# Kernel tuning notes

Measured on AMD Instinct MI355X. Metric: run time of the kernel, lower is better.

The kernel has to match this reference:

```python
import jax, jax.numpy as jnp
import numpy as np

N_NODES = 50000
N_EDGES = 1_600_000
F = 64      # num_edge_features
NH = 3      # n_h hidden blocks
BN_EPS = 1e-5


def setup_inputs() -> dict:
    key = jax.random.key(0)
    ks = jax.random.split(key, 8)
    edge_attr = jax.random.normal(ks[0], (N_EDGES, F), jnp.float32)
    nbr_shift = 0.1 * jax.random.normal(ks[1], (N_EDGES, 3), jnp.float32)
    pos = 10.0 * jax.random.normal(ks[2], (N_NODES, 3), jnp.float32)
    edge_index = jax.random.randint(ks[3], (2, N_EDGES), 0, N_NODES, dtype=jnp.int64)
    Ws = jax.random.normal(ks[4], (NH, F, F), jnp.float32) / np.sqrt(F).astype(np.float32)
    bs = jnp.zeros((NH, F), jnp.float32)
    gammas = jnp.ones((NH, F), jnp.float32)
    betas = jnp.zeros((NH, F), jnp.float32)
    w_out = jax.random.normal(ks[5], (F,), jnp.float32) / np.sqrt(F).astype(np.float32)
    b_out = jnp.zeros((1,), jnp.float32)
    return {"edge_attr": edge_attr, "nbr_shift": nbr_shift, "pos": pos,
            "Ws": Ws, "bs": bs, "gammas": gammas, "betas": betas,
            "w_out": w_out, "b_out": b_out, "edge_index": edge_index}


def _batchnorm(x, gamma, beta):
    # training-mode BatchNorm1d: batch mean / biased variance over edges
    mu = jnp.mean(x, axis=0)
    var = jnp.mean(jnp.square(x - mu), axis=0)
    return gamma * (x - mu) * jax.lax.rsqrt(var + BN_EPS) + beta


def reference(edge_attr, nbr_shift, pos, Ws, bs, gammas, betas, w_out, b_out, edge_index):
    j = edge_index[0]  # source atoms
    i = edge_index[1]  # target atoms
    # gather positions by edge, normalized edge direction  [E,3]
    edge_dir = pos[i] + nbr_shift - pos[j]
    edge_len = jnp.sqrt(jnp.sum(jnp.square(edge_dir), axis=-1, keepdims=True))
    edge_dir = edge_dir / edge_len
    h = edge_attr
    for l in range(NH):
        h = _batchnorm(h @ Ws[l] + bs[l], gammas[l], betas[l])
        h = jax.nn.softplus(h)
    s = (h @ w_out)[:, None] + b_out  # [E,1] scalar per edge
    force_e = s * edge_dir            # [E,3]
    # scatter-add edge forces onto target atoms
    force = jax.ops.segment_sum(force_e, i, num_segments=N_NODES)  # [N,3]
    return force
```

## Files before the change

### kernel.cpp

```cpp
#include <hip/hip_runtime.h>
#include <hip/hip_bf16.h>
#include <math.h>

#define F 64
#define TPB 256
#define MTILE 256
#define BN_EPS 1e-5f
#define LGRID 512

typedef __attribute__((ext_vector_type(8))) short short8;
typedef __attribute__((ext_vector_type(4))) float f32x4;

__device__ __forceinline__ float sp(float x) {
    return fmaxf(x, 0.f) + __logf(1.f + __expf(-fabsf(x)));
}
__device__ __forceinline__ ushort f2bf(float f) {
    __hip_bfloat16 h = __float2bfloat16(f);
    return *reinterpret_cast<ushort*>(&h);
}
__device__ __forceinline__ float bf2f(ushort u) {
    unsigned v = ((unsigned)u) << 16;
    return __builtin_bit_cast(float, v);
}

template <int HAS_ACT>
__global__ __launch_bounds__(TPB, 2)
void layer_mfma(const void* __restrict__ Xv, uint2* __restrict__ Yg,
                const float* __restrict__ W,
                const float* __restrict__ prev_stats,
                const float* __restrict__ gamma_prev,
                const float* __restrict__ beta_prev,
                float* __restrict__ stats_out, int E)
{
    __shared__ short8 Wt[512];
    __shared__ float aca[F], acb[F];
    __shared__ float sh_s[F], sh_q[F];

    const int t  = threadIdx.x;
    const int w  = t >> 6;
    const int l  = t & 63;
    const int ln = l & 15;
    const int q  = l >> 4;

    #pragma unroll
    for (int uu = 0; uu < 2; ++uu) {
        int u = t + uu * 256;
        int kq = u >> 6, n = u & 63;
        short8 pk;
        #pragma unroll
        for (int j = 0; j < 8; ++j)
            pk[j] = (short)f2bf(W[(kq * 8 + j) * F + n]);
        Wt[u] = pk;
    }
    if (t < F) {
        sh_s[t] = 0.f; sh_q[t] = 0.f;
        if (HAS_ACT) {
            float inv_e = 1.f / (float)E;
            float mu = prev_stats[t] * inv_e;
            float var = prev_stats[F + t] * inv_e - mu * mu;
            float a = gamma_prev[t] * rsqrtf(var + BN_EPS);
            aca[t] = a;
            acb[t] = beta_prev[t] - mu * a;
        }
    }
    __syncthreads();

    short8 afr[4][2];
    #pragma unroll
    for (int ni = 0; ni < 4; ++ni)
        #pragma unroll
        for (int ks = 0; ks < 2; ++ks)
            afr[ni][ks] = Wt[(4 * ks + q) * 64 + ni * 16 + ln];

    float ps[16], pq[16];
    #pragma unroll
    for (int p = 0; p < 16; ++p) { ps[p] = 0.f; pq[p] = 0.f; }

    const int ntiles = E >> 8;

    uint2  xb_a[4][2][2];
    float4 xb_f[4][2][2];

    {
        const long e00 = (long)blockIdx.x * MTILE + w * 64;
        #pragma unroll
        for (int mi = 0; mi < 4; ++mi) {
            const long e = e00 + mi * 16 + ln;
            #pragma unroll
            for (int ks = 0; ks < 2; ++ks) {
                if (HAS_ACT) {
                    const uint2* X = (const uint2*)Xv;
                    xb_a[mi][ks][0] = X[(size_t)(8 * ks + 2 * q) * E + e];
                    xb_a[mi][ks][1] = X[(size_t)(8 * ks + 2 * q + 1) * E + e];
                } else {
                    const float4* X4 = (const float4*)Xv;
                    xb_f[mi][ks][0] = X4[(size_t)e * 16 + 8 * ks + 2 * q];
                    xb_f[mi][ks][1] = X4[(size_t)e * 16 + 8 * ks + 2 * q + 1];
                }
            }
        }
    }

    #pragma unroll 1
    for (int tile = blockIdx.x; tile < ntiles; tile += LGRID) {
        const long e0 = (long)tile * MTILE + w * 64;

        short8 bfr[4][2];
        #pragma unroll
        for (int mi = 0; mi < 4; ++mi)
            #pragma unroll
            for (int ks = 0; ks < 2; ++ks) {
                short8 b;
                if (HAS_ACT) {
                    uint vs[4] = {xb_a[mi][ks][0].x, xb_a[mi][ks][0].y,
                                  xb_a[mi][ks][1].x, xb_a[mi][ks][1].y};
                    #pragma unroll
                    for (int d = 0; d < 4; ++d) {
                        float x0 = bf2f((ushort)(vs[d] & 0xffffu));
                        float x1 = bf2f((ushort)(vs[d] >> 16));
                        int k0 = 32 * ks + 8 * q + 2 * d;
                        b[2*d]   = (short)f2bf(sp(aca[k0]     * x0 + acb[k0]));
                        b[2*d+1] = (short)f2bf(sp(aca[k0 + 1] * x1 + acb[k0 + 1]));
                    }
                } else {
                    float4 f0 = xb_f[mi][ks][0], f1 = xb_f[mi][ks][1];
                    b[0] = (short)f2bf(f0.x); b[1] = (short)f2bf(f0.y);
                    b[2] = (short)f2bf(f0.z); b[3] = (short)f2bf(f0.w);
                    b[4] = (short)f2bf(f1.x); b[5] = (short)f2bf(f1.y);
                    b[6] = (short)f2bf(f1.z); b[7] = (short)f2bf(f1.w);
                }
                bfr[mi][ks] = b;
            }

        const int tnext = tile + LGRID;
        if (tnext < ntiles) {
            const long en = (long)tnext * MTILE + w * 64;
            #pragma unroll
            for (int mi = 0; mi < 4; ++mi) {
                const long e = en + mi * 16 + ln;
                #pragma unroll
                for (int ks = 0; ks < 2; ++ks) {
                    if (HAS_ACT) {
                        const uint2* X = (const uint2*)Xv;
                        xb_a[mi][ks][0] = X[(size_t)(8 * ks + 2 * q) * E + e];
                        xb_a[mi][ks][1] = X[(size_t)(8 * ks + 2 * q + 1) * E + e];
                    } else {
                        const float4* X4 = (const float4*)Xv;
                        xb_f[mi][ks][0] = X4[(size_t)e * 16 + 8 * ks + 2 * q];
                        xb_f[mi][ks][1] = X4[(size_t)e * 16 + 8 * ks + 2 * q + 1];
                    }
                }
            }
        }

        f32x4 acc[4][4];
        #pragma unroll
        for (int ni = 0; ni < 4; ++ni)
            #pragma unroll
            for (int mi = 0; mi < 4; ++mi)
                acc[ni][mi] = (f32x4){0.f, 0.f, 0.f, 0.f};

        #pragma unroll
        for (int mi = 0; mi < 4; ++mi)
            #pragma unroll
            for (int ks = 0; ks < 2; ++ks)
                #pragma unroll
                for (int ni = 0; ni < 4; ++ni)
                    acc[ni][mi] = __builtin_amdgcn_mfma_f32_16x16x32_bf16(
                                      afr[ni][ks], bfr[mi][ks], acc[ni][mi], 0, 0, 0);

        #pragma unroll
        for (int ni = 0; ni < 4; ++ni)
            #pragma unroll
            for (int mi = 0; mi < 4; ++mi) {
                const long e = e0 + mi * 16 + ln;
                f32x4 v = acc[ni][mi];
                uint2 u;
                u.x = (uint)f2bf(v[0]) | ((uint)f2bf(v[1]) << 16);
                u.y = (uint)f2bf(v[2]) | ((uint)f2bf(v[3]) << 16);
                Yg[(size_t)(ni * 4 + q) * E + e] = u;
                #pragma unroll
                for (int r = 0; r < 4; ++r) {
                    float x = v[r];
                    ps[ni * 4 + r] += x;
                    pq[ni * 4 + r] = fmaf(x, x, pq[ni * 4 + r]);
                }
            }
    }

    #pragma unroll
    for (int p = 0; p < 16; ++p) {
        #pragma unroll
        for (int m = 1; m < 16; m <<= 1) {
            ps[p] += __shfl_xor(ps[p], m);
            pq[p] += __shfl_xor(pq[p], m);
        }
    }
    if (ln == 0) {
        #pragma unroll
        for (int p = 0; p < 16; ++p) {
            int n = (p >> 2) * 16 + q * 4 + (p & 3);
            atomicAdd(&sh_s[n], ps[p]);
            atomicAdd(&sh_q[n], pq[p]);
        }
    }
    __syncthreads();
    if (t < F) {
        unsafeAtomicAdd(&stats_out[t], sh_s[t]);
        unsafeAtomicAdd(&stats_out[F + t], sh_q[t]);
    }
}

__global__ __launch_bounds__(TPB)
void s_kernel(const uint2* __restrict__ Yg, const float* __restrict__ stats,
              const float* __restrict__ gamma, const float* __restrict__ beta,
              const float* __restrict__ w_out, const float* __restrict__ b_out,
              float* __restrict__ s_out, int E)
{
    __shared__ float ac[2 * F];
    __shared__ float wsh[F];
    const int t = threadIdx.x;
    if (t < F) {
        float inv_e = 1.f / (float)E;
        float mu = stats[t] * inv_e;
        float var = stats[F + t] * inv_e - mu * mu;
        float a = gamma[t] * rsqrtf(var + BN_EPS);
        ac[t] = a;
        ac[F + t] = beta[t] - mu * a;
        wsh[t] = w_out[t];
    }
    __syncthreads();

    const long e = (long)blockIdx.x * TPB + t;
    if (e >= E) return;

    float s = b_out[0];
    #pragma unroll
    for (int nq = 0; nq < 16; ++nq) {
        uint2 u = Yg[(size_t)nq * E + e];
        int k = 4 * nq;
        float x0 = bf2f((ushort)(u.x & 0xffffu));
        float x1 = bf2f((ushort)(u.x >> 16));
        float x2 = bf2f((ushort)(u.y & 0xffffu));
        float x3 = bf2f((ushort)(u.y >> 16));
        s = fmaf(sp(ac[k]     * x0 + ac[F + k]),     wsh[k],     s);
        s = fmaf(sp(ac[k + 1] * x1 + ac[F + k + 1]), wsh[k + 1], s);
        s = fmaf(sp(ac[k + 2] * x2 + ac[F + k + 2]), wsh[k + 2], s);
        s = fmaf(sp(ac[k + 3] * x3 + ac[F + k + 3]), wsh[k + 3], s);
    }
    s_out[e] = s;
}

__global__ __launch_bounds__(TPB)
void force_kernel(const float* __restrict__ s_in,
                  const float* __restrict__ nbr_shift, const float* __restrict__ pos,
                  const int* __restrict__ edge_index, float* __restrict__ out, int E)
{
    const long e = (long)blockIdx.x * TPB + threadIdx.x;
    if (e >= E) return;

    const int jn  = edge_index[e];
    const int in_ = edge_index[E + e];
    float dx = pos[3 * in_ + 0] + nbr_shift[3 * e + 0] - pos[3 * jn + 0];
    float dy = pos[3 * in_ + 1] + nbr_shift[3 * e + 1] - pos[3 * jn + 1];
    float dz = pos[3 * in_ + 2] + nbr_shift[3 * e + 2] - pos[3 * jn + 2];
    float inv = rsqrtf(dx * dx + dy * dy + dz * dz);
    float fs = s_in[e] * inv;
    unsafeAtomicAdd(&out[3 * in_ + 0], fs * dx);
    unsafeAtomicAdd(&out[3 * in_ + 1], fs * dy);
    unsafeAtomicAdd(&out[3 * in_ + 2], fs * dz);
}

extern "C" void kernel_launch(void* const* d_in, const int* in_sizes, int n_in,
                              void* d_out, int out_size, void* d_ws, size_t ws_size,
                              hipStream_t stream)
{
    const int E = in_sizes[0] / F;
    const float* edge_attr = (const float*)d_in[0];
    const float* nbr_shift = (const float*)d_in[1];
    const float* pos       = (const float*)d_in[2];
    const float* Ws        = (const float*)d_in[3];
    const float* gammas    = (const float*)d_in[5];
    const float* betas     = (const float*)d_in[6];
    const float* w_out     = (const float*)d_in[7];
    const float* b_out     = (const float*)d_in[8];
    const int*   edge_index= (const int*)d_in[9];

    uint2* Y1 = (uint2*)d_ws;
    uint2* Y2 = (uint2*)((char*)d_ws + (size_t)E * F * 2);
    float* stats = (float*)((char*)d_ws + (size_t)E * F * 4);
    float* s_buf = (float*)((char*)d_ws + (size_t)E * F * 4 + 4096);

    hipMemsetAsync(stats, 0, 6 * F * sizeof(float), stream);
    hipMemsetAsync(d_out, 0, (size_t)out_size * sizeof(float), stream);

    layer_mfma<0><<<LGRID, TPB, 0, stream>>>(edge_attr, Y1, Ws,
                                             nullptr, nullptr, nullptr, stats, E);
    layer_mfma<1><<<LGRID, TPB, 0, stream>>>(Y1, Y2, Ws + F * F,
                                             stats, gammas, betas, stats + 2 * F, E);
    layer_mfma<1><<<LGRID, TPB, 0, stream>>>(Y2, Y1, Ws + 2 * F * F,
                                             stats + 2 * F, gammas + F, betas + F,
                                             stats + 4 * F, E);
    s_kernel<<<E / TPB, TPB, 0, stream>>>(Y1, stats + 4 * F, gammas + 2 * F,
                                          betas + 2 * F, w_out, b_out, s_buf, E);
    force_kernel<<<E / TPB, TPB, 0, stream>>>(s_buf, nbr_shift, pos, edge_index,
                                              (float*)d_out, E);
}
```

Baseline: 1.069 ms.

## Fuse scalar head into force scatter, replicate atomic targets, double-buffer layer loads

Merges the per-edge scalar head into the force scatter kernel, so the s buffer is no longer written and re-read. The scatter now spreads its atomics across 8 replicated output buffers, chosen by block index, and a small reduction kernel sums them into the output. This cuts atomic contention at the cost of a larger memset and an extra pass. The activated MFMA layers also switch to explicit A/B register double buffering with per-mi conversion, which raises register use.

After: 1.037 ms. -3.0%, faster.

```diff
diff --git a/kernel.cpp b/kernel.cpp
--- a/kernel.cpp
+++ b/kernel.cpp
@@ -7,6 +7,7 @@
 #define MTILE 256
 #define BN_EPS 1e-5f
 #define LGRID 512
+#define NREP 8
 
 typedef __attribute__((ext_vector_type(8))) short short8;
 typedef __attribute__((ext_vector_type(4))) float f32x4;
@@ -78,42 +79,60 @@
 
     const int ntiles = E >> 8;
 
-    uint2  xb_a[4][2][2];
-    float4 xb_f[4][2][2];
-
-    {
-        const long e00 = (long)blockIdx.x * MTILE + w * 64;
-        #pragma unroll
-        for (int mi = 0; mi < 4; ++mi) {
-            const long e = e00 + mi * 16 + ln;
-            #pragma unroll
-            for (int ks = 0; ks < 2; ++ks) {
-                if (HAS_ACT) {
-                    const uint2* X = (const uint2*)Xv;
-                    xb_a[mi][ks][0] = X[(size_t)(8 * ks + 2 * q) * E + e];
-                    xb_a[mi][ks][1] = X[(size_t)(8 * ks + 2 * q + 1) * E + e];
-                } else {
-                    const float4* X4 = (const float4*)Xv;
-                    xb_f[mi][ks][0] = X4[(size_t)e * 16 + 8 * ks + 2 * q];
-                    xb_f[mi][ks][1] = X4[(size_t)e * 16 + 8 * ks + 2 * q + 1];
+    auto store_acc = [&](f32x4 (&acc)[4][4], int tt) {
+        const long e0 = (long)tt * MTILE + w * 64;
+        #pragma unroll
+        for (int ni = 0; ni < 4; ++ni)
+            #pragma unroll
+            for (int mi = 0; mi < 4; ++mi) {
+                const long e = e0 + mi * 16 + ln;
+                f32x4 v = acc[ni][mi];
+                uint2 u;
+                u.x = (uint)f2bf(v[0]) | ((uint)f2bf(v[1]) << 16);
+                u.y = (uint)f2bf(v[2]) | ((uint)f2bf(v[3]) << 16);
+                Yg[(size_t)(ni * 4 + q) * E + e] = u;
+                #pragma unroll
+                for (int r = 0; r < 4; ++r) {
+                    float x = v[r];
+                    ps[ni * 4 + r] += x;
+                    pq[ni * 4 + r] = fmaf(x, x, pq[ni * 4 + r]);
                 }
             }
-        }
-    }
-
-    #pragma unroll 1
-    for (int tile = blockIdx.x; tile < ntiles; tile += LGRID) {
-        const long e0 = (long)tile * MTILE + w * 64;
-
-        short8 bfr[4][2];
-        #pragma unroll
-        for (int mi = 0; mi < 4; ++mi)
-            #pragma unroll
-            for (int ks = 0; ks < 2; ++ks) {
-                short8 b;
-                if (HAS_ACT) {
-                    uint vs[4] = {xb_a[mi][ks][0].x, xb_a[mi][ks][0].y,
-                                  xb_a[mi][ks][1].x, xb_a[mi][ks][1].y};
+    };
+
+    if constexpr (HAS_ACT) {
+        const uint2* X = (const uint2*)Xv;
+        uint2 xbA[4][2][2], xbB[4][2][2];
+
+        auto load = [&](uint2 (&xb)[4][2][2], int tt) {
+            const long eb = (long)tt * MTILE + w * 64;
+            #pragma unroll
+            for (int mi = 0; mi < 4; ++mi) {
+                const long e = eb + mi * 16 + ln;
+                #pragma unroll
+                for (int ks = 0; ks < 2; ++ks) {
+                    xb[mi][ks][0] = X[(size_t)(8 * ks + 2 * q) * E + e];
+                    xb[mi][ks][1] = X[(size_t)(8 * ks + 2 * q + 1) * E + e];
+                }
+            }
+        };
+
+        auto process = [&](uint2 (&xb)[4][2][2], int tt) {
+            f32x4 acc[4][4];
+            #pragma unroll
+            for (int ni = 0; ni < 4; ++ni)
+                #pragma unroll
+                for (int mi = 0; mi < 4; ++mi)
+                    acc[ni][mi] = (f32x4){0.f, 0.f, 0.f, 0.f};
+
+            #pragma unroll
+            for (int mi = 0; mi < 4; ++mi) {
+                short8 bfr[2];
+                #pragma unroll
+                for (int ks = 0; ks < 2; ++ks) {
+                    uint vs[4] = {xb[mi][ks][0].x, xb[mi][ks][0].y,
+                                  xb[mi][ks][1].x, xb[mi][ks][1].y};
+                    short8 b;
                     #pragma unroll
                     for (int d = 0; d < 4; ++d) {
                         float x0 = bf2f((ushort)(vs[d] & 0xffffu));
@@ -122,70 +141,82 @@
                         b[2*d]   = (short)f2bf(sp(aca[k0]     * x0 + acb[k0]));
                         b[2*d+1] = (short)f2bf(sp(aca[k0 + 1] * x1 + acb[k0 + 1]));
                     }
-                } else {
-                    float4 f0 = xb_f[mi][ks][0], f1 = xb_f[mi][ks][1];
+                    bfr[ks] = b;
+                }
+                #pragma unroll
+                for (int ks = 0; ks < 2; ++ks)
+                    #pragma unroll
+                    for (int ni = 0; ni < 4; ++ni)
+                        acc[ni][mi] = __builtin_amdgcn_mfma_f32_16x16x32_bf16(
+                                          afr[ni][ks], bfr[ks], acc[ni][mi], 0, 0, 0);
+            }
+            store_acc(acc, tt);
+        };
+
+        int tile = blockIdx.x;
+        load(xbA, tile);
+        while (true) {
+            const int tB = tile + LGRID;
+            const bool haveB = tB < ntiles;
+            if (haveB) load(xbB, tB);
+            process(xbA, tile);
+            if (!haveB) break;
+            tile = tB + LGRID;
+            if (tile < ntiles) load(xbA, tile);
+            process(xbB, tB);
+            if (tile >= ntiles) break;
+        }
+    } else {
+        const float4* X4 = (const float4*)Xv;
+        float4 xb[4][2][2];
+
+        auto load = [&](int tt) {
+            const long eb = (long)tt * MTILE + w * 64;
+            #pragma unroll
+            for (int mi = 0; mi < 4; ++mi) {
+                const long e = eb + mi * 16 + ln;
+                #pragma unroll
+                for (int ks = 0; ks < 2; ++ks) {
+                    xb[mi][ks][0] = X4[(size_t)e * 16 + 8 * ks + 2 * q];
+                    xb[mi][ks][1] = X4[(size_t)e * 16 + 8 * ks + 2 * q + 1];
+                }
+            }
+        };
+
+        load(blockIdx.x);
+        #pragma unroll 1
+        for (int tile = blockIdx.x; tile < ntiles; tile += LGRID) {
+            short8 bfr[4][2];
+            #pragma unroll
+            for (int mi = 0; mi < 4; ++mi)
+                #pragma unroll
+                for (int ks = 0; ks < 2; ++ks) {
+                    float4 f0 = xb[mi][ks][0], f1 = xb[mi][ks][1];
+                    short8 b;
                     b[0] = (short)f2bf(f0.x); b[1] = (short)f2bf(f0.y);
                     b[2] = (short)f2bf(f0.z); b[3] = (short)f2bf(f0.w);
                     b[4] = (short)f2bf(f1.x); b[5] = (short)f2bf(f1.y);
                     b[6] = (short)f2bf(f1.z); b[7] = (short)f2bf(f1.w);
-                }
-                bfr[mi][ks] = b;
-            }
-
-        const int tnext = tile + LGRID;
-        if (tnext < ntiles) {
-            const long en = (long)tnext * MTILE + w * 64;
-            #pragma unroll
-            for (int mi = 0; mi < 4; ++mi) {
-                const long e = en + mi * 16 + ln;
-                #pragma unroll
-                for (int ks = 0; ks < 2; ++ks) {
-                    if (HAS_ACT) {
-                        const uint2* X = (const uint2*)Xv;
-                        xb_a[mi][ks][0] = X[(size_t)(8 * ks + 2 * q) * E + e];
-                        xb_a[mi][ks][1] = X[(size_t)(8 * ks + 2 * q + 1) * E + e];
-                    } else {
-                        const float4* X4 = (const float4*)Xv;
-                        xb_f[mi][ks][0] = X4[(size_t)e * 16 + 8 * ks + 2 * q];
-                        xb_f[mi][ks][1] = X4[(size_t)e * 16 + 8 * ks + 2 * q + 1];
-                    }
-                }
-            }
-        }
-
-        f32x4 acc[4][4];
-        #pragma unroll
-        for (int ni = 0; ni < 4; ++ni)
+                    bfr[mi][ks] = b;
+                }
+            if (tile + LGRID < ntiles) load(tile + LGRID);
+
+            f32x4 acc[4][4];
+            #pragma unroll
+            for (int ni = 0; ni < 4; ++ni)
+                #pragma unroll
+                for (int mi = 0; mi < 4; ++mi)
+                    acc[ni][mi] = (f32x4){0.f, 0.f, 0.f, 0.f};
             #pragma unroll
             for (int mi = 0; mi < 4; ++mi)
-                acc[ni][mi] = (f32x4){0.f, 0.f, 0.f, 0.f};
-
-        #pragma unroll
-        for (int mi = 0; mi < 4; ++mi)
-            #pragma unroll
-            for (int ks = 0; ks < 2; ++ks)
-                #pragma unroll
-                for (int ni = 0; ni < 4; ++ni)
-                    acc[ni][mi] = __builtin_amdgcn_mfma_f32_16x16x32_bf16(
-                                      afr[ni][ks], bfr[mi][ks], acc[ni][mi], 0, 0, 0);
-
-        #pragma unroll
-        for (int ni = 0; ni < 4; ++ni)
-            #pragma unroll
-            for (int mi = 0; mi < 4; ++mi) {
-                const long e = e0 + mi * 16 + ln;
-                f32x4 v = acc[ni][mi];
-                uint2 u;
-                u.x = (uint)f2bf(v[0]) | ((uint)f2bf(v[1]) << 16);
-                u.y = (uint)f2bf(v[2]) | ((uint)f2bf(v[3]) << 16);
-                Yg[(size_t)(ni * 4 + q) * E + e] = u;
-                #pragma unroll
-                for (int r = 0; r < 4; ++r) {
-                    float x = v[r];
-                    ps[ni * 4 + r] += x;
-                    pq[ni * 4 + r] = fmaf(x, x, pq[ni * 4 + r]);
-                }
-            }
+                #pragma unroll
+                for (int ks = 0; ks < 2; ++ks)
+                    #pragma unroll
+                    for (int ni = 0; ni < 4; ++ni)
+                        acc[ni][mi] = __builtin_amdgcn_mfma_f32_16x16x32_bf16(
+                                          afr[ni][ks], bfr[mi][ks], acc[ni][mi], 0, 0, 0);
+            store_acc(acc, tile);
+        }
     }
 
     #pragma unroll
@@ -212,10 +243,12 @@
 }
 
 __global__ __launch_bounds__(TPB)
-void s_kernel(const uint2* __restrict__ Yg, const float* __restrict__ stats,
-              const float* __restrict__ gamma, const float* __restrict__ beta,
-              const float* __restrict__ w_out, const float* __restrict__ b_out,
-              float* __restrict__ s_out, int E)
+void force_kernel(const uint2* __restrict__ Yg, const float* __restrict__ stats,
+                  const float* __restrict__ gamma, const float* __restrict__ beta,
+                  const float* __restrict__ w_out, const float* __restrict__ b_out,
+                  const float* __restrict__ nbr_shift, const float* __restrict__ pos,
+                  const int* __restrict__ edge_index, float* __restrict__ rep,
+                  int E, int nodes3)
 {
     __shared__ float ac[2 * F];
     __shared__ float wsh[F];
@@ -248,16 +281,6 @@
         s = fmaf(sp(ac[k + 2] * x2 + ac[F + k + 2]), wsh[k + 2], s);
         s = fmaf(sp(ac[k + 3] * x3 + ac[F + k + 3]), wsh[k + 3], s);
     }
-    s_out[e] = s;
-}
-
-__global__ __launch_bounds__(TPB)
-void force_kernel(const float* __restrict__ s_in,
-                  const float* __restrict__ nbr_shift, const float* __restrict__ pos,
-                  const int* __restrict__ edge_index, float* __restrict__ out, int E)
-{
-    const long e = (long)blockIdx.x * TPB + threadIdx.x;
-    if (e >= E) return;
 
     const int jn  = edge_index[e];
     const int in_ = edge_index[E + e];
@@ -265,10 +288,24 @@
     float dy = pos[3 * in_ + 1] + nbr_shift[3 * e + 1] - pos[3 * jn + 1];
     float dz = pos[3 * in_ + 2] + nbr_shift[3 * e + 2] - pos[3 * jn + 2];
     float inv = rsqrtf(dx * dx + dy * dy + dz * dz);
-    float fs = s_in[e] * inv;
-    unsafeAtomicAdd(&out[3 * in_ + 0], fs * dx);
-    unsafeAtomicAdd(&out[3 * in_ + 1], fs * dy);
-    unsafeAtomicAdd(&out[3 * in_ + 2], fs * dz);
+    float fs = s * inv;
+
+    float* myrep = rep + (size_t)(blockIdx.x & (NREP - 1)) * nodes3;
+    unsafeAtomicAdd(&myrep[3 * in_ + 0], fs * dx);
+    unsafeAtomicAdd(&myrep[3 * in_ + 1], fs * dy);
+    unsafeAtomicAdd(&myrep[3 * in_ + 2], fs * dz);
+}
+
+__global__ __launch_bounds__(TPB)
+void reduce_out(const float* __restrict__ rep, float* __restrict__ out, int nodes3)
+{
+    const int i = blockIdx.x * TPB + threadIdx.x;
+    if (i >= nodes3) return;
+    float s = 0.f;
+    #pragma unroll
+    for (int r = 0; r < NREP; ++r)
+        s += rep[(size_t)r * nodes3 + i];
+    out[i] = s;
 }
 
 extern "C" void kernel_launch(void* const* d_in, const int* in_sizes, int n_in,
@@ -289,10 +326,10 @@
     uint2* Y1 = (uint2*)d_ws;
     uint2* Y2 = (uint2*)((char*)d_ws + (size_t)E * F * 2);
     float* stats = (float*)((char*)d_ws + (size_t)E * F * 4);
-    float* s_buf = (float*)((char*)d_ws + (size_t)E * F * 4 + 4096);
+    float* rep   = (float*)((char*)d_ws + (size_t)E * F * 4 + 4096);
 
     hipMemsetAsync(stats, 0, 6 * F * sizeof(float), stream);
-    hipMemsetAsync(d_out, 0, (size_t)out_size * sizeof(float), stream);
+    hipMemsetAsync(rep, 0, (size_t)NREP * out_size * sizeof(float), stream);
 
     layer_mfma<0><<<LGRID, TPB, 0, stream>>>(edge_attr, Y1, Ws,
                                              nullptr, nullptr, nullptr, stats, E);
@@ -301,8 +338,10 @@
     layer_mfma<1><<<LGRID, TPB, 0, stream>>>(Y2, Y1, Ws + 2 * F * F,
                                              stats + 2 * F, gammas + F, betas + F,
                                              stats + 4 * F, E);
-    s_kernel<<<E / TPB, TPB, 0, stream>>>(Y1, stats + 4 * F, gammas + 2 * F,
-                                          betas + 2 * F, w_out, b_out, s_buf, E);
-    force_kernel<<<E / TPB, TPB, 0, stream>>>(s_buf, nbr_shift, pos, edge_index,
-                                              (float*)d_out, E);
-}
+    force_kernel<<<E / TPB, TPB, 0, stream>>>(Y1, stats + 4 * F, gammas + 2 * F,
+                                              betas + 2 * F, w_out, b_out,
+                                              nbr_shift, pos, edge_index, rep,
+                                              E, out_size);
+    reduce_out<<<(out_size + TPB - 1) / TPB, TPB, 0, stream>>>(rep, (float*)d_out,
+                                                               out_size);
+}
```
